# Optimization experiments

Measured on AMD Instinct MI355X. Metric: run time of the kernel, lower is better.

## Reference

```python
import jax, jax.numpy as jnp
import numpy as np

B, N, D = 2, 2048, 1024          # batch, seq (= wh*ww), model dim
H, HD = 16, 64                   # heads, head_dim (inner_dim = H*HD = D)
MLP = 4096                       # SwiGLU hidden dim
WSY, WSX = 16, 32                # ws_y = wh//2, ws_x = ww//2  (wh=32, ww=64)
EPS = float(jnp.finfo(jnp.float32).eps)  # torch RMSNorm default eps


def setup_inputs() -> dict:
    key = jax.random.key(0)
    ks = jax.random.split(key, 8)
    return {
        "x": jax.random.normal(ks[0], (B, N, D), jnp.float32),
        "t": jax.random.normal(ks[1], (B,), jnp.float32),
        "dt": jax.random.normal(ks[2], (B, D), jnp.float32),
        "w_qkv": (jax.random.normal(ks[3], (3 * H * HD, D), jnp.float32) * 0.02),
        "w_o": (jax.random.normal(ks[4], (D, H * HD), jnp.float32) * 0.02),
        "w1": (jax.random.normal(ks[5], (2 * MLP, D), jnp.float32) * 0.02),
        "w2": (jax.random.normal(ks[6], (D, MLP), jnp.float32) * 0.02),
        "g_attn": jnp.ones((D,), jnp.float32),  # RMSNorm weight (attn)
        "g_ff": jnp.ones((D,), jnp.float32),    # RMSNorm weight (ffn)
    }


def _rms(x, g):
    return x * jax.lax.rsqrt(jnp.mean(x * x, axis=-1, keepdims=True) + EPS) * g


def _win(x):
    # 'b h (wc_y wc_x ws_y ws_x) d' -> 'b h (wc_y ws_y wc_x ws_x) d'
    b, h, n, d = x.shape
    return x.reshape(b, h, 2, 2, WSY, WSX, d).transpose(0, 1, 2, 4, 3, 5, 6).reshape(b, h, n, d)


def _unwin(x):
    # inverse of _win
    b, h, n, d = x.shape
    return x.reshape(b, h, 2, WSY, 2, WSX, d).transpose(0, 1, 2, 4, 3, 5, 6).reshape(b, h, n, d)


def reference(x, t, dt, w_qkv, w_o, w1, w2, g_attn, g_ff):
    # ---- SPAttention (pre-norm); all-to-all is identity on 1 device ----
    h = _rms(x, g_attn)
    qkv = h @ w_qkv.T                              # [B,N,3*H*HD]
    q, k, v = jnp.split(qkv, 3, axis=-1)
    as_heads = lambda z: z.reshape(B, N, H, HD).transpose(0, 2, 1, 3)  # b h n d
    q, k, v = _win(as_heads(q)), _win(as_heads(k)), _win(as_heads(v))
    # NOTE: the source computes RoPE2D(q), RoPE2D(k) but discards the result;
    # attention consumes the UNROTATED seq_gathered_q/k/v. Faithful: no rotation.
    scale = 1.0 / jnp.sqrt(jnp.float32(HD))        # SDPA default scale
    s = jnp.einsum('bhqd,bhkd->bhqk', q, k) * scale
    a = jax.nn.softmax(s, axis=-1)
    o = jnp.einsum('bhqk,bhkd->bhqd', a, v)
    o = _unwin(o).transpose(0, 2, 1, 3).reshape(B, N, H * HD)
    x = x + o @ w_o.T                               # residual
    # ---- SwiGLU FeedForward (pre-norm) + residual ----
    hf = _rms(x, g_ff)
    gate, up = jnp.split(hf @ w1.T, 2, axis=-1)
    return x + (jax.nn.silu(gate) * up) @ w2.T
```

## Files before the change

### kernel.cpp

```cpp
#include <hip/hip_runtime.h>
#include <cstdint>
#include <cstddef>

typedef __attribute__((ext_vector_type(8)))  __bf16 bf16x8;
typedef __attribute__((ext_vector_type(4)))  __bf16 bf16x4;
typedef __attribute__((ext_vector_type(4)))  float  f32x4;
typedef __attribute__((ext_vector_type(16))) float  f32x16;
typedef __attribute__((ext_vector_type(2)))  uint32_t u32x2;
typedef __attribute__((ext_vector_type(4)))  uint32_t u32x4;

#define MFMA_BF16(a, b, c) __builtin_amdgcn_mfma_f32_16x16x32_bf16((a), (b), (c), 0, 0, 0)
#define MFMA32(a, b, c)    __builtin_amdgcn_mfma_f32_32x32x16_bf16((a), (b), (c), 0, 0, 0)

__device__ __forceinline__ void gload_lds16(const __bf16* src, __bf16* lds_dst) {
    __builtin_amdgcn_global_load_lds(
        (const __attribute__((address_space(1))) void*)(const_cast<__bf16*>(src)),
        (__attribute__((address_space(3))) void*)(lds_dst), 16, 0, 0);
}

__device__ __forceinline__ uint32_t pack2(float a, float b) {
    uint16_t ua = __builtin_bit_cast(uint16_t, (__bf16)a);
    uint16_t ub = __builtin_bit_cast(uint16_t, (__bf16)b);
    return (uint32_t)ua | ((uint32_t)ub << 16);
}

__global__ __launch_bounds__(256) void cvt_kernel(const float* __restrict__ src,
                                                  __bf16* __restrict__ dst) {
    int i = blockIdx.x * 256 + threadIdx.x;
    float4 v = reinterpret_cast<const float4*>(src)[i];
    bf16x4 o;
    o[0] = (__bf16)v.x; o[1] = (__bf16)v.y; o[2] = (__bf16)v.z; o[3] = (__bf16)v.w;
    reinterpret_cast<bf16x4*>(dst)[i] = o;
}

__global__ __launch_bounds__(256) void rmsnorm_kernel(const float* __restrict__ x,
                                                      const float* __restrict__ g,
                                                      __bf16* __restrict__ out) {
    const int row = blockIdx.x;
    const int t = threadIdx.x;
    float4 v = reinterpret_cast<const float4*>(x + (size_t)row * 1024)[t];
    float ss = v.x * v.x + v.y * v.y + v.z * v.z + v.w * v.w;
#pragma unroll
    for (int m = 1; m < 64; m <<= 1) ss += __shfl_xor(ss, m);
    __shared__ float sred[4];
    if ((t & 63) == 0) sred[t >> 6] = ss;
    __syncthreads();
    float tot = sred[0] + sred[1] + sred[2] + sred[3];
    float rs = rsqrtf(tot * (1.0f / 1024.0f) + 1.1920928955078125e-07f);
    float4 gv = reinterpret_cast<const float4*>(g)[t];
    bf16x4 o;
    o[0] = (__bf16)(v.x * rs * gv.x);
    o[1] = (__bf16)(v.y * rs * gv.y);
    o[2] = (__bf16)(v.z * rs * gv.z);
    o[3] = (__bf16)(v.w * rs * gv.w);
    *reinterpret_cast<bf16x4*>(out + (size_t)row * 1024 + t * 4) = o;
}

template <int MODE, int NB>
__global__ __launch_bounds__(256) void gemm_nt(const __bf16* __restrict__ A, int lda,
                                               const __bf16* __restrict__ B, int ldb,
                                               __bf16* __restrict__ outb,
                                               float* __restrict__ outf,
                                               const float* __restrict__ resid,
                                               int K, int ldo) {
    constexpr int BN = NB * 32;
    __shared__ __attribute__((aligned(16))) __bf16 As[128 * 64];
    __shared__ __attribute__((aligned(16))) __bf16 Bs[BN * 64];
    const int t = threadIdx.x;
    const int lane = t & 63;
    const int wid = t >> 6;
    const int bm = blockIdx.x, bn = blockIdx.y;
    const int wm = (wid >> 1) * 64, wn = (wid & 1) * (NB * 16);
    f32x4 acc[4][NB] = {};

    for (int kt = 0; kt < K; kt += 64) {
        __syncthreads();
#pragma unroll
        for (int i = 0; i < 4; ++i) {
            int L = i * 256 + t;
            int r = L >> 3, s = L & 7;
            int c = s ^ (r & 7);
            gload_lds16(A + (size_t)(bm * 128 + r) * lda + kt + c * 8, As + L * 8);
        }
#pragma unroll
        for (int i = 0; i < NB; ++i) {
            int L = i * 256 + t;
            int r = L >> 3, s = L & 7;
            int c = s ^ (r & 7);
            int rb = bn * BN + r;
            int srow = (MODE == 2) ? ((rb >> 1) + ((rb & 1) << 12)) : rb;
            gload_lds16(B + (size_t)srow * ldb + kt + c * 8, Bs + L * 8);
        }
        __syncthreads();
#pragma unroll
        for (int ks = 0; ks < 2; ++ks) {
            bf16x8 af[4], bfr[NB];
#pragma unroll
            for (int mi = 0; mi < 4; ++mi) {
                int r = wm + mi * 16 + (lane & 15);
                int slot = (ks * 4 + (lane >> 4)) ^ (r & 7);
                af[mi] = *reinterpret_cast<const bf16x8*>(As + r * 64 + slot * 8);
            }
#pragma unroll
            for (int ni = 0; ni < NB; ++ni) {
                int r = wn + ni * 16 + (lane & 15);
                int slot = (ks * 4 + (lane >> 4)) ^ (r & 7);
                bfr[ni] = *reinterpret_cast<const bf16x8*>(Bs + r * 64 + slot * 8);
            }
#pragma unroll
            for (int mi = 0; mi < 4; ++mi)
#pragma unroll
                for (int ni = 0; ni < NB; ++ni)
                    acc[mi][ni] = MFMA_BF16(af[mi], bfr[ni], acc[mi][ni]);
        }
    }
    const int row0 = bm * 128 + wm + ((lane >> 4) << 2);
    const int col0 = bn * BN + wn + (lane & 15);
#pragma unroll
    for (int mi = 0; mi < 4; ++mi)
#pragma unroll
        for (int ni = 0; ni < NB; ++ni)
#pragma unroll
            for (int r2 = 0; r2 < 4; ++r2) {
                int row = row0 + mi * 16 + r2;
                int col = col0 + ni * 16;
                float v = acc[mi][ni][r2];
                if (MODE == 0) {
                    outb[(size_t)row * ldo + col] = (__bf16)v;
                } else if (MODE == 1) {
                    size_t idx = (size_t)row * ldo + col;
                    outf[idx] = v + resid[idx];
                } else {
                    float pv = __shfl_xor(v, 1);
                    if (!(lane & 1)) {
                        float sg = v / (1.0f + __expf(-v));
                        outb[(size_t)row * ldo + (col >> 1)] = (__bf16)(sg * pv);
                    }
                }
            }
}

__global__ __launch_bounds__(256) void vtrans_kernel(const __bf16* __restrict__ qkv,
                                                     __bf16* __restrict__ vt) {
    __shared__ __bf16 T[64][68];
    const int t = threadIdx.x;
    const int bh = blockIdx.y, b = bh >> 4, h = bh & 15;
    const int n0 = blockIdx.x * 64;
    const __bf16* vp = qkv + (size_t)b * 2048 * 3072 + 2048 + h * 64;
#pragma unroll
    for (int i = 0; i < 2; ++i) {
        int r = i * 32 + (t >> 3), c = t & 7;
        bf16x8 v = *reinterpret_cast<const bf16x8*>(vp + (size_t)(n0 + r) * 3072 + c * 8);
#pragma unroll
        for (int j = 0; j < 8; ++j) T[c * 8 + j][r] = v[j];
    }
    __syncthreads();
#pragma unroll
    for (int i = 0; i < 2; ++i) {
        int hd = i * 32 + (t >> 3), c = t & 7;
        bf16x8 v;
#pragma unroll
        for (int j = 0; j < 8; ++j) v[j] = T[hd][c * 8 + j];
        *reinterpret_cast<bf16x8*>(vt + ((size_t)bh * 64 + hd) * 2048 + n0 + c * 8) = v;
    }
}

__global__ __launch_bounds__(256) void attn_kernel(const __bf16* __restrict__ qkv,
                                                   const __bf16* __restrict__ vt,
                                                   __bf16* __restrict__ o) {
    __shared__ __attribute__((aligned(16))) __bf16 Ks[2][128 * 64];
    __shared__ __attribute__((aligned(16))) __bf16 Vs[2][64 * 128];
    const int t = threadIdx.x;
    const int lane = t & 63;
    const int w = t >> 6;
    const int hi = lane >> 5;
    const int l31 = lane & 31;
    const int bh = blockIdx.y;
    const int b = bh >> 4, h = bh & 15;
    const __bf16* qp = qkv + (size_t)b * 2048 * 3072 + h * 64;
    const __bf16* kp = qp + 1024;
    const __bf16* vtp = vt + (size_t)bh * 64 * 2048;
    const int q0 = blockIdx.x * 128 + w * 32;

    const float SC = 0.18033688011112042f;
    bf16x8 qf[4];
#pragma unroll
    for (int s = 0; s < 4; ++s) {
        bf16x8 raw = *reinterpret_cast<const bf16x8*>(
            qp + (size_t)(q0 + l31) * 3072 + s * 16 + hi * 8);
        bf16x8 sc;
#pragma unroll
        for (int j = 0; j < 8; ++j) sc[j] = (__bf16)((float)raw[j] * SC);
        qf[s] = sc;
    }

    f32x16 oa[2] = {};
    float m_run = -INFINITY, l_run = 0.0f;

    auto stage = [&](int buf, int kt) {
#pragma unroll
        for (int i = 0; i < 4; ++i) {
            int L = i * 256 + t;
            int r = L >> 3, s = L & 7;
            int c = s ^ (r & 7);
            gload_lds16(kp + (size_t)(kt + r) * 3072 + c * 8, &Ks[buf][L * 8]);
        }
#pragma unroll
        for (int i = 0; i < 4; ++i) {
            int L = i * 256 + t;
            int r = L >> 4, s = L & 15;
            int c = s ^ (r & 15);
            gload_lds16(vtp + (size_t)r * 2048 + kt + c * 8, &Vs[buf][L * 8]);
        }
    };
    stage(0, 0);
    __syncthreads();

    for (int kt = 0; kt < 2048; kt += 128) {
        const int buf = (kt >> 7) & 1;
        if (kt + 128 < 2048) stage(buf ^ 1, kt + 128);

#pragma unroll
        for (int h2 = 0; h2 < 2; ++h2) {
            f32x16 st[2] = {};
#pragma unroll
            for (int s = 0; s < 4; ++s) {
#pragma unroll
                for (int mb = 0; mb < 2; ++mb) {
                    int r = h2 * 64 + mb * 32 + l31;
                    int sl = (s * 2 + hi) ^ (r & 7);
                    bf16x8 kf = *reinterpret_cast<const bf16x8*>(&Ks[buf][r * 64 + sl * 8]);
                    st[mb] = MFMA32(kf, qf[s], st[mb]);
                }
            }
            float mt = -INFINITY;
#pragma unroll
            for (int mb = 0; mb < 2; ++mb)
#pragma unroll
                for (int r = 0; r < 16; ++r) mt = fmaxf(mt, st[mb][r]);
            mt = fmaxf(mt, __shfl_xor(mt, 32));
            if (__any(mt > m_run + 8.0f)) {
                float m_new = fmaxf(m_run, mt);
                float alpha = exp2f(m_run - m_new);
#pragma unroll
                for (int r = 0; r < 16; ++r) {
                    float av = __shfl(alpha, (r & 3) + 8 * (r >> 2) + 4 * hi);
                    oa[0][r] *= av;
                    oa[1][r] *= av;
                }
                l_run *= alpha;
                m_run = m_new;
            }
            float ps = 0.0f;
#pragma unroll
            for (int mb = 0; mb < 2; ++mb)
#pragma unroll
                for (int r = 0; r < 16; ++r) {
                    float p = exp2f(st[mb][r] - m_run);
                    st[mb][r] = p;
                    ps += p;
                }
            ps += __shfl_xor(ps, 32);
            l_run += ps;

            uint32_t pk[16];
#pragma unroll
            for (int mb = 0; mb < 2; ++mb)
#pragma unroll
                for (int i2 = 0; i2 < 8; ++i2)
                    pk[mb * 8 + i2] = pack2(st[mb][2 * i2], st[mb][2 * i2 + 1]);

#pragma unroll
            for (int s2 = 0; s2 < 4; ++s2) {
                const int I0 = (s2 >> 1) * 8 + (s2 & 1) * 4;
                u32x2 w02 = __builtin_amdgcn_permlane32_swap(pk[I0], pk[I0 + 2], false, false);
                u32x2 w13 = __builtin_amdgcn_permlane32_swap(pk[I0 + 1], pk[I0 + 3], false, false);
                u32x4 fv;
                fv[0] = w02[0]; fv[1] = w13[0]; fv[2] = w02[1]; fv[3] = w13[1];
                bf16x8 pa = __builtin_bit_cast(bf16x8, fv);
#pragma unroll
                for (int nb = 0; nb < 2; ++nb) {
                    int rv = nb * 32 + l31;
                    int ch = h2 * 8 + s2 * 2 + hi;
                    int sl = ch ^ (rv & 15);
                    bf16x8 vf = *reinterpret_cast<const bf16x8*>(&Vs[buf][rv * 128 + sl * 8]);
                    oa[nb] = MFMA32(pa, vf, oa[nb]);
                }
            }
        }
        __syncthreads();
    }

#pragma unroll
    for (int r = 0; r < 16; ++r) {
        int crow = (r & 3) + 8 * (r >> 2) + 4 * hi;
        float lv = __shfl(l_run, crow);
        float inv = 1.0f / lv;
        int row = q0 + crow;
        size_t base = ((size_t)b * 2048 + row) * 1024 + h * 64 + l31;
        o[base]      = (__bf16)(oa[0][r] * inv);
        o[base + 32] = (__bf16)(oa[1][r] * inv);
    }
}

extern "C" void kernel_launch(void* const* d_in, const int* in_sizes, int n_in,
                              void* d_out, int out_size, void* d_ws, size_t ws_size,
                              hipStream_t stream) {
    const float* x      = (const float*)d_in[0];
    const float* w_qkv  = (const float*)d_in[3];
    const float* w_o    = (const float*)d_in[4];
    const float* w1     = (const float*)d_in[5];
    const float* w2     = (const float*)d_in[6];
    const float* g_attn = (const float*)d_in[7];
    const float* g_ff   = (const float*)d_in[8];
    float* out = (float*)d_out;

    char* ws = (char*)d_ws;
    size_t off = 0;
    auto alloc = [&](size_t bytes) -> void* {
        void* p = ws + off;
        off += (bytes + 255) & ~(size_t)255;
        return p;
    };
    __bf16* wqkv_b = (__bf16*)alloc((size_t)3072 * 1024 * 2);
    __bf16* wo_b   = (__bf16*)alloc((size_t)1024 * 1024 * 2);
    __bf16* w1_b   = (__bf16*)alloc((size_t)8192 * 1024 * 2);
    __bf16* w2_b   = (__bf16*)alloc((size_t)1024 * 4096 * 2);
    __bf16* h_b    = (__bf16*)alloc((size_t)4096 * 1024 * 2);
    __bf16* qkv_b  = (__bf16*)alloc((size_t)4096 * 3072 * 2);
    __bf16* o_b    = (__bf16*)alloc((size_t)4096 * 1024 * 2);
    float*  x2     = (float*)alloc((size_t)4096 * 1024 * 4);
    __bf16* vt_b   = (__bf16*)alloc((size_t)32 * 64 * 2048 * 2);
    __bf16* act_b  = qkv_b;

    cvt_kernel<<<3072, 256, 0, stream>>>(w_qkv, wqkv_b);
    cvt_kernel<<<1024, 256, 0, stream>>>(w_o, wo_b);
    cvt_kernel<<<8192, 256, 0, stream>>>(w1, w1_b);
    cvt_kernel<<<4096, 256, 0, stream>>>(w2, w2_b);

    rmsnorm_kernel<<<4096, 256, 0, stream>>>(x, g_attn, h_b);
    gemm_nt<0, 4><<<dim3(32, 24), 256, 0, stream>>>(h_b, 1024, wqkv_b, 1024,
                                                    qkv_b, nullptr, nullptr, 1024, 3072);
    vtrans_kernel<<<dim3(32, 32), 256, 0, stream>>>(qkv_b, vt_b);
    attn_kernel<<<dim3(16, 32), 256, 0, stream>>>(qkv_b, vt_b, o_b);
    gemm_nt<1, 2><<<dim3(32, 16), 256, 0, stream>>>(o_b, 1024, wo_b, 1024,
                                                    nullptr, x2, x, 1024, 1024);
    rmsnorm_kernel<<<4096, 256, 0, stream>>>(x2, g_ff, h_b);
    gemm_nt<2, 4><<<dim3(32, 64), 256, 0, stream>>>(h_b, 1024, w1_b, 1024,
                                                    act_b, nullptr, nullptr, 1024, 4096);
    gemm_nt<1, 2><<<dim3(32, 16), 256, 0, stream>>>(act_b, 4096, w2_b, 4096,
                                                    nullptr, out, x2, 4096, 1024);
}
```

Before: 320.2 us.

## Add triple-buffered 256x128 MFMA32 GEMM for QKV and gated W1 projections

Adds a new GEMM kernel with 512 threads, 256x128 tiles, a three-stage LDS ring buffer that keeps global-to-LDS loads two tiles ahead, and 32x32x16 MFMA instructions. It is used for the QKV projection and the SwiGLU W1 projection (with the fused silu-gate epilogue). The old kernel loses its MODE 2 path. The aim is to hide global load latency and raise data reuse per tile. In exchange it uses much more LDS (about 144 KB per block) and more registers, which limits occupancy.

```diff
diff --git a/kernel.cpp b/kernel.cpp
--- a/kernel.cpp
+++ b/kernel.cpp
@@ -54,6 +54,125 @@
     o[2] = (__bf16)(v.z * rs * gv.z);
     o[3] = (__bf16)(v.w * rs * gv.w);
     *reinterpret_cast<bf16x4*>(out + (size_t)row * 1024 + t * 4) = o;
+}
+
+template <int MODE>
+__global__ __launch_bounds__(512, 2) void gemm_pipe(const __bf16* __restrict__ A, int lda,
+                                                    const __bf16* __restrict__ B, int ldb,
+                                                    __bf16* __restrict__ outb,
+                                                    int K, int ldo) {
+    __shared__ __attribute__((aligned(16))) __bf16 As[3][256 * 64];
+    __shared__ __attribute__((aligned(16))) __bf16 Bs[3][128 * 64];
+    const int t = threadIdx.x;
+    const int lane = t & 63;
+    const int wid = t >> 6;
+    const int l31 = lane & 31;
+    const int hi = lane >> 5;
+    const int bm = blockIdx.x, bn = blockIdx.y;
+    const int wm = (wid >> 1) * 64;
+    const int wn = (wid & 1) * 64;
+
+    const __bf16* aptr[4];
+    const __bf16* bptr[2];
+#pragma unroll
+    for (int i = 0; i < 4; ++i) {
+        int L = i * 512 + t; int r = L >> 3; int c = (L & 7) ^ (r & 7);
+        aptr[i] = A + (size_t)(bm * 256 + r) * lda + c * 8;
+    }
+#pragma unroll
+    for (int i = 0; i < 2; ++i) {
+        int L = i * 512 + t; int r = L >> 3; int c = (L & 7) ^ (r & 7);
+        int rb = bn * 128 + r;
+        int srow = (MODE == 2) ? ((rb >> 1) + ((rb & 1) << 12)) : rb;
+        bptr[i] = B + (size_t)srow * ldb + c * 8;
+    }
+
+    auto stage = [&](int buf) {
+#pragma unroll
+        for (int i = 0; i < 4; ++i) {
+            gload_lds16(aptr[i], &As[buf][(i * 512 + t) * 8]);
+            aptr[i] += 64;
+        }
+#pragma unroll
+        for (int i = 0; i < 2; ++i) {
+            gload_lds16(bptr[i], &Bs[buf][(i * 512 + t) * 8]);
+            bptr[i] += 64;
+        }
+    };
+
+    const int e = l31 & 7;
+    int aoff[2][4], boff[2][4];
+#pragma unroll
+    for (int mi = 0; mi < 2; ++mi)
+#pragma unroll
+        for (int ks = 0; ks < 4; ++ks)
+            aoff[mi][ks] = (wm + mi * 32 + l31) * 128 + (((ks * 2 + hi) ^ e) * 16);
+#pragma unroll
+    for (int ni = 0; ni < 2; ++ni)
+#pragma unroll
+        for (int ks = 0; ks < 4; ++ks)
+            boff[ni][ks] = (wn + ni * 32 + l31) * 128 + (((ks * 2 + hi) ^ e) * 16);
+
+    f32x16 acc[2][2] = {};
+
+    const int NT = K >> 6;
+    stage(0);
+    stage(1);
+    asm volatile("s_waitcnt vmcnt(6)\n\ts_barrier" ::: "memory");
+
+    int buf = 0;
+    for (int kt = 0; kt < NT; ++kt) {
+        const char* abase = (const char*)&As[buf][0];
+        const char* bbase = (const char*)&Bs[buf][0];
+        bf16x8 af[2][4], bfr[2][4];
+#pragma unroll
+        for (int mi = 0; mi < 2; ++mi)
+#pragma unroll
+            for (int ks = 0; ks < 4; ++ks)
+                af[mi][ks] = *reinterpret_cast<const bf16x8*>(abase + aoff[mi][ks]);
+#pragma unroll
+        for (int ni = 0; ni < 2; ++ni)
+#pragma unroll
+            for (int ks = 0; ks < 4; ++ks)
+                bfr[ni][ks] = *reinterpret_cast<const bf16x8*>(bbase + boff[ni][ks]);
+        int nbuf = buf + 2; if (nbuf >= 3) nbuf -= 3;
+        if (kt + 2 < NT) stage(nbuf);
+#pragma unroll
+        for (int ks = 0; ks < 4; ++ks)
+#pragma unroll
+            for (int mi = 0; mi < 2; ++mi)
+#pragma unroll
+                for (int ni = 0; ni < 2; ++ni)
+                    acc[mi][ni] = MFMA32(af[mi][ks], bfr[ni][ks], acc[mi][ni]);
+        if (kt + 2 < NT) {
+            asm volatile("s_waitcnt vmcnt(6)\n\ts_barrier" ::: "memory");
+        } else {
+            asm volatile("s_waitcnt vmcnt(0)\n\ts_barrier" ::: "memory");
+        }
+        buf += 1; if (buf >= 3) buf = 0;
+    }
+
+    const int row0 = bm * 256 + wm + 4 * hi;
+    const int col0 = bn * 128 + wn + l31;
+#pragma unroll
+    for (int mi = 0; mi < 2; ++mi)
+#pragma unroll
+        for (int ni = 0; ni < 2; ++ni)
+#pragma unroll
+            for (int r = 0; r < 16; ++r) {
+                int row = row0 + mi * 32 + (r & 3) + 8 * (r >> 2);
+                int col = col0 + ni * 32;
+                float v = acc[mi][ni][r];
+                if (MODE == 0) {
+                    outb[(size_t)row * ldo + col] = (__bf16)v;
+                } else {
+                    float pv = __shfl_xor(v, 1);
+                    if (!(l31 & 1)) {
+                        float sg = v / (1.0f + __expf(-v));
+                        outb[(size_t)row * ldo + (col >> 1)] = (__bf16)(sg * pv);
+                    }
+                }
+            }
 }
 
 template <int MODE, int NB>
@@ -88,8 +207,7 @@
             int r = L >> 3, s = L & 7;
             int c = s ^ (r & 7);
             int rb = bn * BN + r;
-            int srow = (MODE == 2) ? ((rb >> 1) + ((rb & 1) << 12)) : rb;
-            gload_lds16(B + (size_t)srow * ldb + kt + c * 8, Bs + L * 8);
+            gload_lds16(B + (size_t)rb * ldb + kt + c * 8, Bs + L * 8);
         }
         __syncthreads();
 #pragma unroll
@@ -127,15 +245,9 @@
                 float v = acc[mi][ni][r2];
                 if (MODE == 0) {
                     outb[(size_t)row * ldo + col] = (__bf16)v;
-                } else if (MODE == 1) {
+                } else {
                     size_t idx = (size_t)row * ldo + col;
                     outf[idx] = v + resid[idx];
-                } else {
-                    float pv = __shfl_xor(v, 1);
-                    if (!(lane & 1)) {
-                        float sg = v / (1.0f + __expf(-v));
-                        outb[(size_t)row * ldo + (col >> 1)] = (__bf16)(sg * pv);
-                    }
                 }
             }
 }
@@ -339,15 +451,15 @@
     cvt_kernel<<<4096, 256, 0, stream>>>(w2, w2_b);
 
     rmsnorm_kernel<<<4096, 256, 0, stream>>>(x, g_attn, h_b);
-    gemm_nt<0, 4><<<dim3(32, 24), 256, 0, stream>>>(h_b, 1024, wqkv_b, 1024,
-                                                    qkv_b, nullptr, nullptr, 1024, 3072);
+    gemm_pipe<0><<<dim3(16, 24), 512, 0, stream>>>(h_b, 1024, wqkv_b, 1024,
+                                                   qkv_b, 1024, 3072);
     vtrans_kernel<<<dim3(32, 32), 256, 0, stream>>>(qkv_b, vt_b);
     attn_kernel<<<dim3(16, 32), 256, 0, stream>>>(qkv_b, vt_b, o_b);
     gemm_nt<1, 2><<<dim3(32, 16), 256, 0, stream>>>(o_b, 1024, wo_b, 1024,
                                                     nullptr, x2, x, 1024, 1024);
     rmsnorm_kernel<<<4096, 256, 0, stream>>>(x2, g_ff, h_b);
-    gemm_nt<2, 4><<<dim3(32, 64), 256, 0, stream>>>(h_b, 1024, w1_b, 1024,
-                                                    act_b, nullptr, nullptr, 1024, 4096);
+    gemm_pipe<2><<<dim3(16, 64), 512, 0, stream>>>(h_b, 1024, w1_b, 1024,
+                                                   act_b, 1024, 4096);
     gemm_nt<1, 2><<<dim3(32, 16), 256, 0, stream>>>(act_b, 4096, w2_b, 4096,
                                                     nullptr, out, x2, 4096, 1024);
 }
```

New measurement: 337.2 us. 5.3% more time.

## Add 256x256 8-wave ping-pong pipelined GEMM for QKV and W1 projections

Applied to the files above, without the earlier changes.

Adds a new gemm_8p kernel with 512 threads, 256x256 tiles and an 8-slot LDS ring of half-K stages. Global-to-LDS loads for later stages are interleaved with MFMA blocks, separated by barriers and raised wave priority. It replaces the 128-tile gemm_nt for the QKV and fused SwiGLU W1 GEMMs, aiming for more data reuse per tile and better load/compute overlap. The trade-offs are a large LDS footprint, high register pressure from 128 accumulators per thread, and fewer blocks in the grid.

```diff
diff --git a/kernel.cpp b/kernel.cpp
--- a/kernel.cpp
+++ b/kernel.cpp
@@ -22,6 +22,10 @@
     uint16_t ua = __builtin_bit_cast(uint16_t, (__bf16)a);
     uint16_t ub = __builtin_bit_cast(uint16_t, (__bf16)b);
     return (uint32_t)ua | ((uint32_t)ub << 16);
+}
+
+__device__ __forceinline__ bf16x8 ldv(const void* p) {
+    return *reinterpret_cast<const bf16x8*>(p);
 }
 
 __global__ __launch_bounds__(256) void cvt_kernel(const float* __restrict__ src,
@@ -54,6 +58,157 @@
     o[2] = (__bf16)(v.z * rs * gv.z);
     o[3] = (__bf16)(v.w * rs * gv.w);
     *reinterpret_cast<bf16x4*>(out + (size_t)row * 1024 + t * 4) = o;
+}
+
+template <int MODE>
+__global__ __launch_bounds__(512, 2) void gemm_8p(const __bf16* __restrict__ A, int lda,
+                                                  const __bf16* __restrict__ B, int ldb,
+                                                  __bf16* __restrict__ outb,
+                                                  int K, int ldo) {
+    __shared__ __attribute__((aligned(16))) __bf16 Sl[8][256 * 32];
+    const int t = threadIdx.x;
+    const int lane = t & 63;
+    const int wid = t >> 6;
+    const int l15 = lane & 15;
+    const int g4 = lane >> 4;
+    const int bm = blockIdx.x, bn = blockIdx.y;
+    const int wm = (wid >> 2) * 128;
+    const int wn = (wid & 3) * 64;
+
+    const __bf16 *pa[2], *pb[2];
+#pragma unroll
+    for (int i = 0; i < 2; ++i) {
+        int L = i * 512 + t, r = L >> 2, c = (L & 3) ^ ((r >> 1) & 3);
+        pa[i] = A + (size_t)(bm * 256 + r) * lda + c * 8;
+        int rb = bn * 256 + r;
+        int srow = (MODE == 2) ? ((rb >> 1) + ((rb & 1) << 12)) : rb;
+        pb[i] = B + (size_t)srow * ldb + c * 8;
+    }
+    auto stageA = [&](int slot) {
+#pragma unroll
+        for (int i = 0; i < 2; ++i) {
+            gload_lds16(pa[i], &Sl[slot][(i * 512 + t) * 8]);
+            pa[i] += 32;
+        }
+    };
+    auto stageB = [&](int slot) {
+#pragma unroll
+        for (int i = 0; i < 2; ++i) {
+            gload_lds16(pb[i], &Sl[slot][(i * 512 + t) * 8]);
+            pb[i] += 32;
+        }
+    };
+
+    int aoff[8], boff[4];
+#pragma unroll
+    for (int m = 0; m < 8; ++m) {
+        int r = wm + m * 16 + l15;
+        aoff[m] = r * 64 + ((g4 ^ ((r >> 1) & 3)) * 16);
+    }
+#pragma unroll
+    for (int n = 0; n < 4; ++n) {
+        int r = wn + n * 16 + l15;
+        boff[n] = r * 64 + ((g4 ^ ((r >> 1) & 3)) * 16);
+    }
+
+    f32x4 acc[8][4] = {};
+    const int NT = K >> 6;
+
+    stageA(0); stageB(1); stageA(2); stageB(3); stageA(4); stageB(5);
+    asm volatile("s_waitcnt vmcnt(4)" ::: "memory");
+    __builtin_amdgcn_s_barrier();
+
+    for (int tt = 0; tt < NT; ++tt) {
+        const int q = (tt & 1) * 4, nq = q ^ 4;
+        const char* Alo = (const char*)&Sl[q + 0][0];
+        const char* Blo = (const char*)&Sl[q + 1][0];
+        const char* Ahi = (const char*)&Sl[q + 2][0];
+        const char* Bhi = (const char*)&Sl[q + 3][0];
+        bf16x8 af[4], bf[4];
+
+#pragma unroll
+        for (int m = 0; m < 4; ++m) af[m] = ldv(Alo + aoff[m]);
+#pragma unroll
+        for (int n = 0; n < 4; ++n) bf[n] = ldv(Blo + boff[n]);
+        if (tt + 1 < NT) stageA(nq + 2);
+        __builtin_amdgcn_s_barrier();
+        __builtin_amdgcn_s_setprio(1);
+#pragma unroll
+        for (int m = 0; m < 4; ++m)
+#pragma unroll
+            for (int n = 0; n < 4; ++n)
+                acc[m][n] = MFMA_BF16(af[m], bf[n], acc[m][n]);
+        __builtin_amdgcn_s_setprio(0);
+        __builtin_amdgcn_s_barrier();
+
+#pragma unroll
+        for (int m = 0; m < 4; ++m) af[m] = ldv(Alo + aoff[4 + m]);
+        if (tt + 1 < NT) stageB(nq + 3);
+        __builtin_amdgcn_s_barrier();
+        __builtin_amdgcn_s_setprio(1);
+#pragma unroll
+        for (int m = 0; m < 4; ++m)
+#pragma unroll
+            for (int n = 0; n < 4; ++n)
+                acc[4 + m][n] = MFMA_BF16(af[m], bf[n], acc[4 + m][n]);
+        __builtin_amdgcn_s_setprio(0);
+        __builtin_amdgcn_s_barrier();
+
+#pragma unroll
+        for (int m = 0; m < 4; ++m) af[m] = ldv(Ahi + aoff[m]);
+#pragma unroll
+        for (int n = 0; n < 4; ++n) bf[n] = ldv(Bhi + boff[n]);
+        if (tt + 2 < NT) stageA(q + 0);
+        __builtin_amdgcn_s_barrier();
+        __builtin_amdgcn_s_setprio(1);
+#pragma unroll
+        for (int m = 0; m < 4; ++m)
+#pragma unroll
+            for (int n = 0; n < 4; ++n)
+                acc[m][n] = MFMA_BF16(af[m], bf[n], acc[m][n]);
+        __builtin_amdgcn_s_setprio(0);
+        __builtin_amdgcn_s_barrier();
+
+#pragma unroll
+        for (int m = 0; m < 4; ++m) af[m] = ldv(Ahi + aoff[4 + m]);
+        if (tt + 2 < NT) stageB(q + 1);
+        __builtin_amdgcn_s_barrier();
+        __builtin_amdgcn_s_setprio(1);
+#pragma unroll
+        for (int m = 0; m < 4; ++m)
+#pragma unroll
+            for (int n = 0; n < 4; ++n)
+                acc[4 + m][n] = MFMA_BF16(af[m], bf[n], acc[4 + m][n]);
+        __builtin_amdgcn_s_setprio(0);
+        if (tt + 2 < NT) {
+            asm volatile("s_waitcnt vmcnt(4)" ::: "memory");
+        } else {
+            asm volatile("s_waitcnt vmcnt(0)" ::: "memory");
+        }
+        __builtin_amdgcn_s_barrier();
+    }
+
+    const int row0 = bm * 256 + wm + (g4 << 2);
+    const int col0 = bn * 256 + wn + l15;
+#pragma unroll
+    for (int m = 0; m < 8; ++m)
+#pragma unroll
+        for (int n = 0; n < 4; ++n)
+#pragma unroll
+            for (int r2 = 0; r2 < 4; ++r2) {
+                int row = row0 + m * 16 + r2;
+                int col = col0 + n * 16;
+                float v = acc[m][n][r2];
+                if (MODE == 0) {
+                    outb[(size_t)row * ldo + col] = (__bf16)v;
+                } else {
+                    float pv = __shfl_xor(v, 1);
+                    if (!(l15 & 1)) {
+                        float sg = v / (1.0f + __expf(-v));
+                        outb[(size_t)row * ldo + (col >> 1)] = (__bf16)(sg * pv);
+                    }
+                }
+            }
 }
 
 template <int MODE, int NB>
@@ -88,8 +243,7 @@
             int r = L >> 3, s = L & 7;
             int c = s ^ (r & 7);
             int rb = bn * BN + r;
-            int srow = (MODE == 2) ? ((rb >> 1) + ((rb & 1) << 12)) : rb;
-            gload_lds16(B + (size_t)srow * ldb + kt + c * 8, Bs + L * 8);
+            gload_lds16(B + (size_t)rb * ldb + kt + c * 8, Bs + L * 8);
         }
         __syncthreads();
 #pragma unroll
@@ -127,15 +281,9 @@
                 float v = acc[mi][ni][r2];
                 if (MODE == 0) {
                     outb[(size_t)row * ldo + col] = (__bf16)v;
-                } else if (MODE == 1) {
+                } else {
                     size_t idx = (size_t)row * ldo + col;
                     outf[idx] = v + resid[idx];
-                } else {
-                    float pv = __shfl_xor(v, 1);
-                    if (!(lane & 1)) {
-                        float sg = v / (1.0f + __expf(-v));
-                        outb[(size_t)row * ldo + (col >> 1)] = (__bf16)(sg * pv);
-                    }
                 }
             }
 }
@@ -339,15 +487,15 @@
     cvt_kernel<<<4096, 256, 0, stream>>>(w2, w2_b);
 
     rmsnorm_kernel<<<4096, 256, 0, stream>>>(x, g_attn, h_b);
-    gemm_nt<0, 4><<<dim3(32, 24), 256, 0, stream>>>(h_b, 1024, wqkv_b, 1024,
-                                                    qkv_b, nullptr, nullptr, 1024, 3072);
+    gemm_8p<0><<<dim3(16, 12), 512, 0, stream>>>(h_b, 1024, wqkv_b, 1024,
+                                                 qkv_b, 1024, 3072);
     vtrans_kernel<<<dim3(32, 32), 256, 0, stream>>>(qkv_b, vt_b);
     attn_kernel<<<dim3(16, 32), 256, 0, stream>>>(qkv_b, vt_b, o_b);
     gemm_nt<1, 2><<<dim3(32, 16), 256, 0, stream>>>(o_b, 1024, wo_b, 1024,
                                                     nullptr, x2, x, 1024, 1024);
     rmsnorm_kernel<<<4096, 256, 0, stream>>>(x2, g_ff, h_b);
-    gemm_nt<2, 4><<<dim3(32, 64), 256, 0, stream>>>(h_b, 1024, w1_b, 1024,
-                                                    act_b, nullptr, nullptr, 1024, 4096);
+    gemm_8p<2><<<dim3(16, 32), 512, 0, stream>>>(h_b, 1024, w1_b, 1024,
+                                                 act_b, 1024, 4096);
     gemm_nt<1, 2><<<dim3(32, 16), 256, 0, stream>>>(act_b, 4096, w2_b, 4096,
                                                     nullptr, out, x2, 4096, 1024);
 }
```

New measurement: 321.3 us. Within noise of the previous version (+0.3%).
